# Kernel tuning notes

Hardware: AMD Instinct MI355X
Metric: run time of the kernel (lower is better)

The kernel has to match this reference:

```python
import jax, jax.numpy as jnp
import numpy as np

B, T, DIM, FF, E, TOPK = 2, 2048, 1024, 4096, 8, 2


def setup_inputs() -> dict:
    key = jax.random.key(0)
    k0, k1, k2, k3 = jax.random.split(key, 4)
    x = jax.random.normal(k0, (B, T, DIM), jnp.float32)
    # router weight [E, D] (nn.Linear(dim, num_experts, bias=False))
    Wr = jax.random.normal(k1, (E, DIM), jnp.float32) * (DIM ** -0.5)
    # per-expert FFN weights, stacked: W1 [E, D, FF], W2 [E, FF, D]
    W1 = jax.random.normal(k2, (E, DIM, FF), jnp.float32) * (DIM ** -0.5)
    W2 = jax.random.normal(k3, (E, FF, DIM), jnp.float32) * (FF ** -0.5)
    return {"x": x, "Wr": Wr, "W1": W1, "W2": W2}


def reference(x, Wr, W1, W2):
    """MoEFeedForward.forward, world_size=1, STANDARD implementation.

    Math: per token, top_k experts by router logits, softmax over the top_k
    logits (fp32), y = sum_k w_k * FFN_{e_k}(x). The torch code realizes this
    via sort/permute + per-expert variable-size GEMM + weighted index_add;
    the scatter-add result is identical to the dense masked form below,
    which is the jit-friendly (static-shape) expression.
    """
    Bn, Tn, D = x.shape
    num_experts = Wr.shape[0]
    xf = x.reshape(-1, D)                      # [N, D], N = B*T
    N = xf.shape[0]

    logits = xf @ Wr.T                         # [N, E]
    topw, topi = jax.lax.top_k(logits, TOPK)   # [N, K]
    topw = jax.nn.softmax(topw.astype(jnp.float32), axis=-1).astype(x.dtype)

    # combine weight for each (token, expert): [N, E] (0 if not routed)
    combine = jnp.zeros((N, num_experts), x.dtype)
    combine = combine.at[jnp.arange(N)[:, None], topi].add(topw)

    out = jnp.zeros_like(xf)
    for e in range(num_experts):               # fixed small loop over experts
        h = jax.nn.gelu(xf @ W1[e], approximate=False)  # exact GELU (nn.GELU)
        out = out + combine[:, e:e + 1] * (h @ W2[e])
    return out.reshape(Bn, Tn, D)
```

## Files before the change

### kernel.cpp

```cpp
#include <hip/hip_runtime.h>
#include <hip/hip_bf16.h>
#include <hip/hip_fp16.h>

#define NTOK 4096
#define DIM 1024
#define FF 4096
#define NE 8
#define NSLOT 8192

typedef _Float16 half8 __attribute__((ext_vector_type(8)));
typedef _Float16 half4 __attribute__((ext_vector_type(4)));
typedef float floatx4 __attribute__((ext_vector_type(4)));

__device__ __forceinline__ float gelu_exact(float x) {
    return 0.5f * x * (1.0f + erff(x * 0.70710678118654752f));
}

__device__ __forceinline__ void gl_lds16(const void* g, void* l) {
    __builtin_amdgcn_global_load_lds(
        (const __attribute__((address_space(1))) void*)g,
        (__attribute__((address_space(3))) void*)l, 16, 0, 0);
}

__global__ __launch_bounds__(256) void k_convert_x(const float* __restrict__ x,
                                                   _Float16* __restrict__ xh) {
    int i = (blockIdx.x * 256 + threadIdx.x) * 8;
    float4 a = *(const float4*)(x + i);
    float4 b = *(const float4*)(x + i + 4);
    half8 h;
    h[0] = (_Float16)a.x; h[1] = (_Float16)a.y; h[2] = (_Float16)a.z; h[3] = (_Float16)a.w;
    h[4] = (_Float16)b.x; h[5] = (_Float16)b.y; h[6] = (_Float16)b.z; h[7] = (_Float16)b.w;
    *(half8*)(xh + i) = h;
}

template<typename LdsT>
__device__ __forceinline__ void transpose_tile(const float* __restrict__ s,
                                               _Float16* __restrict__ d,
                                               int R, int C, int r0, int c0,
                                               LdsT* ldsraw) {
    float (*t)[65] = (float (*)[65])ldsraw;
    int tid = threadIdx.x;
    int rr = tid >> 4, cc = (tid & 15) * 4;
#pragma unroll
    for (int i = 0; i < 4; ++i) {
        float4 v = *(const float4*)(s + (size_t)(r0 + rr + i * 16) * C + c0 + cc);
        t[rr + i * 16][cc] = v.x; t[rr + i * 16][cc + 1] = v.y;
        t[rr + i * 16][cc + 2] = v.z; t[rr + i * 16][cc + 3] = v.w;
    }
    __syncthreads();
    int f = tid >> 3, ch = tid & 7;
#pragma unroll
    for (int j = 0; j < 2; ++j) {
        int fr = f + j * 32;
        half8 v;
#pragma unroll
        for (int u = 0; u < 8; ++u) v[u] = (_Float16)t[ch * 8 + u][fr];
        *(half8*)(d + (size_t)(c0 + fr) * R + r0 + ch * 8) = v;
    }
}

__global__ __launch_bounds__(256) void k_transpose(const float* __restrict__ src,
                                                   _Float16* __restrict__ dst,
                                                   int R, int C) {
    __shared__ float t[64][65];
    int e = blockIdx.z;
    transpose_tile(src + (size_t)e * R * C, dst + (size_t)e * C * R,
                   R, C, blockIdx.y * 64, blockIdx.x * 64, &t[0][0]);
}

__global__ __launch_bounds__(256) void k_router(const float* __restrict__ x,
                                                const float* __restrict__ Wr,
                                                int* __restrict__ counts,
                                                int* __restrict__ tok_e,
                                                float* __restrict__ tok_w,
                                                int* __restrict__ tok_pos) {
    __shared__ float wr[NE * DIM];
    int tid = threadIdx.x;
    for (int i = tid; i < NE * DIM / 4; i += 256)
        ((float4*)wr)[i] = ((const float4*)Wr)[i];
    __syncthreads();

    int w = tid >> 6, lane = tid & 63;
    int t = blockIdx.x * 4 + w;

    float acc[NE] = {};
    for (int j = 0; j < DIM / 64; ++j) {
        float xv = x[t * DIM + j * 64 + lane];
#pragma unroll
        for (int e = 0; e < NE; ++e)
            acc[e] += xv * wr[e * DIM + j * 64 + lane];
    }
#pragma unroll
    for (int e = 0; e < NE; ++e) {
#pragma unroll
        for (int s = 32; s; s >>= 1) acc[e] += __shfl_xor(acc[e], s, 64);
    }
    if (lane == 0) {
        int b0 = 0; float m0 = acc[0];
#pragma unroll
        for (int e = 1; e < NE; ++e) { if (acc[e] > m0) { m0 = acc[e]; b0 = e; } }
        int b1 = -1; float m1 = -1e30f;
#pragma unroll
        for (int e = 0; e < NE; ++e) { if (e != b0 && acc[e] > m1) { m1 = acc[e]; b1 = e; } }
        float z = __expf(m1 - m0);
        float zz = 1.0f / (1.0f + z);
        int p0 = atomicAdd(&counts[b0], 1);
        int p1 = atomicAdd(&counts[b1], 1);
        tok_e[2 * t] = b0;  tok_e[2 * t + 1] = b1;
        tok_w[2 * t] = zz;  tok_w[2 * t + 1] = z * zz;
        tok_pos[2 * t] = p0; tok_pos[2 * t + 1] = p1;
    }
}

__global__ void k_prefix(const int* __restrict__ counts, int* __restrict__ offs,
                         int* __restrict__ tmap256, int* __restrict__ tmap128) {
    if (threadIdx.x == 0 && blockIdx.x == 0) {
        int s = 0, n2 = 0, n1 = 0;
        for (int e = 0; e < NE; ++e) {
            offs[e] = s;
            int c = counts[e];
            for (int mt = 0; mt * 256 < c; ++mt) tmap256[1 + n2++] = (e << 16) | mt;
            for (int mt = 0; mt * 128 < c; ++mt) tmap128[1 + n1++] = (e << 16) | mt;
            s += c;
        }
        offs[NE] = s;
        tmap256[0] = n2;
        tmap128[0] = n1;
    }
}

__global__ __launch_bounds__(256) void k_slots(const int* __restrict__ offs,
                                               const int* __restrict__ tok_e,
                                               const int* __restrict__ tok_pos,
                                               int* __restrict__ tok_slot,
                                               int* __restrict__ list_tok) {
    int idx = blockIdx.x * 256 + threadIdx.x;
    if (idx < NSLOT) {
        int e = tok_e[idx];
        int slot = offs[e] + tok_pos[idx];
        tok_slot[idx] = slot;
        list_tok[slot] = idx >> 1;
    }
}

template<int K, int NOUT, bool GATHER, bool GELU>
__device__ __forceinline__ void ffn128_body(
    const _Float16* __restrict__ Abase,
    const _Float16* __restrict__ Wbase,
    const int* __restrict__ counts,
    const int* __restrict__ offs,
    const int* __restrict__ list_tok,
    _Float16* __restrict__ Out,
    int e, int mt, int f0, _Float16* lds) {

    int base = offs[e] + mt * 128;
    int valid = counts[e] - mt * 128;

    int tid = threadIdx.x;
    int wid = tid >> 6, lane = tid & 63;

    const char* AB = (const char*)Abase;
    const char* WB = (const char*)(Wbase + (size_t)e * NOUT * K);

    size_t aoff[4]; unsigned boff[4];
#pragma unroll
    for (int i = 0; i < 4; ++i) {
        int g = wid * 256 + i * 64 + lane;
        int r = g >> 3;
        int c = (g & 7) ^ (r & 7);
        int rr = (r < valid) ? r : (valid - 1);
        unsigned arow = GATHER ? (unsigned)list_tok[base + rr] : (unsigned)(base + rr);
        aoff[i] = (size_t)arow * (K * 2) + c * 16;
        boff[i] = (unsigned)(f0 + r) * (unsigned)(K * 2) + c * 16;
    }

    floatx4 acc[4][4];
#pragma unroll
    for (int m = 0; m < 4; ++m)
#pragma unroll
        for (int n = 0; n < 4; ++n) acc[m][n] = (floatx4){0.f, 0.f, 0.f, 0.f};

    int la = lane & 15, lb = lane >> 4;
    int wm = (wid >> 1) * 64, wn = (wid & 1) * 64;

#pragma unroll
    for (int i = 0; i < 4; ++i)
        gl_lds16(AB + aoff[i], lds + wid * 2048 + i * 512);
#pragma unroll
    for (int i = 0; i < 4; ++i)
        gl_lds16(WB + boff[i], lds + 16384 + wid * 2048 + i * 512);
    asm volatile("s_waitcnt vmcnt(0)" ::: "memory");
    __builtin_amdgcn_s_barrier();
    __builtin_amdgcn_sched_barrier(0);

    constexpr int NT = K / 64;
#pragma unroll 2
    for (int t = 0; t < NT; ++t) {
        int cur = t & 1;
        if (t + 1 < NT) {
            size_t kadv = (size_t)(t + 1) * 128;
            _Float16* Ad = lds + (cur ^ 1) * 8192;
            _Float16* Bd = lds + 16384 + (cur ^ 1) * 8192;
#pragma unroll
            for (int i = 0; i < 4; ++i)
                gl_lds16(AB + aoff[i] + kadv, Ad + wid * 2048 + i * 512);
#pragma unroll
            for (int i = 0; i < 4; ++i)
                gl_lds16(WB + boff[i] + kadv, Bd + wid * 2048 + i * 512);
        }
        const _Float16* Ac = lds + cur * 8192;
        const _Float16* Bc = lds + 16384 + cur * 8192;
#pragma unroll
        for (int kk = 0; kk < 2; ++kk) {
            half8 af[4], bf[4];
#pragma unroll
            for (int m = 0; m < 4; ++m) {
                int row = wm + m * 16 + la;
                int c = kk * 4 + lb;
                af[m] = *(const half8*)(Ac + row * 64 + ((c ^ (row & 7)) * 8));
            }
#pragma unroll
            for (int n = 0; n < 4; ++n) {
                int row = wn + n * 16 + la;
                int c = kk * 4 + lb;
                bf[n] = *(const half8*)(Bc + row * 64 + ((c ^ (row & 7)) * 8));
            }
#pragma unroll
            for (int m = 0; m < 4; ++m)
#pragma unroll
                for (int n = 0; n < 4; ++n)
                    acc[m][n] = __builtin_amdgcn_mfma_f32_16x16x32_f16(af[m], bf[n], acc[m][n], 0, 0, 0);
        }
        __builtin_amdgcn_sched_barrier(0);
        asm volatile("s_waitcnt vmcnt(0)" ::: "memory");
        __builtin_amdgcn_s_barrier();
        __builtin_amdgcn_sched_barrier(0);
    }

    _Float16* tw = lds + wid * 4096;
#pragma unroll
    for (int m = 0; m < 4; ++m)
#pragma unroll
        for (int n = 0; n < 4; ++n) {
            floatx4 v = acc[m][n];
#pragma unroll
            for (int i = 0; i < 4; ++i) {
                float fv = v[i];
                if (GELU) fv = gelu_exact(fv);
                tw[(m * 16 + lb * 4 + i) * 64 + n * 16 + la] = (_Float16)fv;
            }
        }
    asm volatile("s_waitcnt lgkmcnt(0)" ::: "memory");
    __builtin_amdgcn_sched_barrier(0);
#pragma unroll
    for (int i = 0; i < 8; ++i) {
        int gi = i * 64 + lane;
        int row = gi >> 3, c8 = gi & 7;
        half8 v = *(const half8*)(tw + gi * 8);
        int trow = wm + row;
        if (trow < valid)
            *(half8*)(Out + (size_t)(base + trow) * NOUT + f0 + wn + c8 * 8) = v;
    }
}

template<int K, int NOUT, bool GATHER, bool GELU>
__global__ __launch_bounds__(256) void k_ffn(
    const _Float16* __restrict__ Abase,
    const _Float16* __restrict__ Wbase,
    const int* __restrict__ tmap,
    const int* __restrict__ counts,
    const int* __restrict__ offs,
    const int* __restrict__ list_tok,
    _Float16* __restrict__ Out) {
    __shared__ _Float16 lds[32768];
    int nt_m = tmap[0];
    if ((int)blockIdx.x >= nt_m) return;
    int ent = tmap[1 + blockIdx.x];
    ffn128_body<K, NOUT, GATHER, GELU>(Abase, Wbase, counts, offs, list_tok, Out,
                                       ent >> 16, ent & 0xffff, blockIdx.y * 128, lds);
}

__global__ __launch_bounds__(256) void k_ffn1_fused(
    const _Float16* __restrict__ xh,
    const _Float16* __restrict__ w1t,
    const int* __restrict__ tmap,
    const int* __restrict__ counts,
    const int* __restrict__ offs,
    const int* __restrict__ list_tok,
    _Float16* __restrict__ hbuf,
    const float* __restrict__ W2,
    _Float16* __restrict__ w2t) {
    __shared__ _Float16 lds[32768];
    int bid = blockIdx.x;
    int q = bid / 9, r = bid % 9;
    if (r < 2) {
        int f = q * 2 + r;
        int nt_m = tmap[0];
        int tile = f >> 5;
        if (tile >= nt_m) return;
        int ent = tmap[1 + tile];
        ffn128_body<DIM, FF, true, true>(xh, w1t, counts, offs, list_tok, hbuf,
                                         ent >> 16, ent & 0xffff, (f & 31) * 128, lds);
    } else {
        int t = q * 7 + (r - 2);
        if (t >= 16 * 64 * NE) return;
        int e = t >> 10, rem = t & 1023;
        int cx = rem & 15, ry = rem >> 4;
        transpose_tile(W2 + (size_t)e * FF * DIM, w2t + (size_t)e * DIM * FF,
                       FF, DIM, ry * 64, cx * 64, (float*)lds);
    }
}

template<int K, int NOUT, int KSPAN, bool GATHER, bool GELU>
__global__ __launch_bounds__(512, 2) void k_ffn256(
    const _Float16* __restrict__ Abase,
    const _Float16* __restrict__ Wbase,
    const int* __restrict__ tmap,
    const int* __restrict__ counts,
    const int* __restrict__ offs,
    const int* __restrict__ list_tok,
    _Float16* __restrict__ Out) {

    int nt_m = tmap[0];
    if ((int)blockIdx.x >= nt_m) return;
    int ent = tmap[1 + blockIdx.x];
    int e = ent >> 16, mt = ent & 0xffff;
    int base = offs[e] + mt * 256;
    int valid = counts[e] - mt * 256;
    int f0 = blockIdx.y * 256;
    int kbase = blockIdx.z * KSPAN;
    Out += (size_t)blockIdx.z * ((size_t)NSLOT * NOUT);

    __shared__ _Float16 lds[65536];

    int tid = threadIdx.x;
    int wid = tid >> 6, lane = tid & 63;

    const char* AB = (const char*)Abase;
    const char* WB = (const char*)(Wbase + (size_t)e * NOUT * K);

    size_t aoff[4]; unsigned boff[4];
#pragma unroll
    for (int i = 0; i < 4; ++i) {
        int g = i * 512 + tid;
        int r = g >> 3;
        int c = (g & 7) ^ (r & 7);
        int rr = (r < valid) ? r : (valid - 1);
        unsigned arow = GATHER ? (unsigned)list_tok[base + rr] : (unsigned)(base + rr);
        aoff[i] = (size_t)arow * (K * 2) + c * 16 + (size_t)kbase * 2;
        boff[i] = (unsigned)(f0 + r) * (unsigned)(K * 2) + c * 16 + (unsigned)kbase * 2;
    }

    floatx4 acc[8][4];
#pragma unroll
    for (int m = 0; m < 8; ++m)
#pragma unroll
        for (int n = 0; n < 4; ++n) acc[m][n] = (floatx4){0.f, 0.f, 0.f, 0.f};

    int la = lane & 15, lb = lane >> 4;
    int wmb = (wid >> 2) * 128, wnb = (wid & 3) * 64;

#pragma unroll
    for (int i = 0; i < 4; ++i)
        gl_lds16(AB + aoff[i], lds + i * 4096 + wid * 512);
#pragma unroll
    for (int i = 0; i < 4; ++i)
        gl_lds16(WB + boff[i], lds + 32768 + i * 4096 + wid * 512);
    asm volatile("s_waitcnt vmcnt(0)" ::: "memory");
    __builtin_amdgcn_s_barrier();
    __builtin_amdgcn_sched_barrier(0);

    constexpr int NT = KSPAN / 64;
#pragma unroll 2
    for (int t = 0; t < NT; ++t) {
        int cur = t & 1;
        if (t + 1 < NT) {
            size_t adv = (size_t)(t + 1) * 128;
            _Float16* Ad = lds + (cur ^ 1) * 16384;
            _Float16* Bd = lds + 32768 + (cur ^ 1) * 16384;
#pragma unroll
            for (int i = 0; i < 4; ++i)
                gl_lds16(AB + aoff[i] + adv, Ad + i * 4096 + wid * 512);
#pragma unroll
            for (int i = 0; i < 4; ++i)
                gl_lds16(WB + boff[i] + adv, Bd + i * 4096 + wid * 512);
        }
        const _Float16* Ac = lds + cur * 16384;
        const _Float16* Bc = lds + 32768 + cur * 16384;
#pragma unroll
        for (int kk = 0; kk < 2; ++kk) {
            half8 af[8], bf[4];
#pragma unroll
            for (int n = 0; n < 4; ++n) {
                int row = wnb + n * 16 + la;
                int c = kk * 4 + lb;
                bf[n] = *(const half8*)(Bc + row * 64 + ((c ^ (row & 7)) * 8));
            }
#pragma unroll
            for (int m = 0; m < 8; ++m) {
                int row = wmb + m * 16 + la;
                int c = kk * 4 + lb;
                af[m] = *(const half8*)(Ac + row * 64 + ((c ^ (row & 7)) * 8));
            }
#pragma unroll
            for (int m = 0; m < 8; ++m)
#pragma unroll
                for (int n = 0; n < 4; ++n)
                    acc[m][n] = __builtin_amdgcn_mfma_f32_16x16x32_f16(af[m], bf[n], acc[m][n], 0, 0, 0);
        }
        __builtin_amdgcn_sched_barrier(0);
        asm volatile("s_waitcnt vmcnt(0)" ::: "memory");
        __builtin_amdgcn_s_barrier();
        __builtin_amdgcn_sched_barrier(0);
    }

    _Float16* tw = lds + wid * 4096;
#pragma unroll
    for (int ps = 0; ps < 2; ++ps) {
#pragma unroll
        for (int fi = 0; fi < 4; ++fi)
#pragma unroll
            for (int nf = 0; nf < 4; ++nf) {
                floatx4 v = acc[ps * 4 + fi][nf];
#pragma unroll
                for (int i2 = 0; i2 < 4; ++i2) {
                    float fv = v[i2];
                    if (GELU) fv = gelu_exact(fv);
                    tw[(fi * 16 + lb * 4 + i2) * 64 + nf * 16 + la] = (_Float16)fv;
                }
            }
        asm volatile("s_waitcnt lgkmcnt(0)" ::: "memory");
        __builtin_amdgcn_sched_barrier(0);
#pragma unroll
        for (int i2 = 0; i2 < 8; ++i2) {
            int gi = i2 * 64 + lane;
            int row = gi >> 3, c8 = gi & 7;
            half8 v = *(const half8*)(tw + gi * 8);
            int trow = wmb + ps * 64 + row;
            if (trow < valid)
                *(half8*)(Out + (size_t)(base + trow) * NOUT + f0 + wnb + c8 * 8) = v;
        }
    }
}

__global__ __launch_bounds__(256) void k_combine(const _Float16* __restrict__ yp,
                                                 const int* __restrict__ tok_slot,
                                                 const float* __restrict__ tok_w,
                                                 float* __restrict__ out,
                                                 int nsplit) {
    int t = blockIdx.x;
    int d = threadIdx.x * 4;
    int s0 = tok_slot[2 * t], s1 = tok_slot[2 * t + 1];
    float w0 = tok_w[2 * t], w1 = tok_w[2 * t + 1];
    float4 sum0 = {0.f, 0.f, 0.f, 0.f}, sum1 = {0.f, 0.f, 0.f, 0.f};
    for (int z = 0; z < nsplit; ++z) {
        const _Float16* p = yp + (size_t)z * NSLOT * DIM;
        half4 y0 = *(const half4*)(p + (size_t)s0 * DIM + d);
        half4 y1 = *(const half4*)(p + (size_t)s1 * DIM + d);
        sum0.x += (float)y0[0]; sum0.y += (float)y0[1];
        sum0.z += (float)y0[2]; sum0.w += (float)y0[3];
        sum1.x += (float)y1[0]; sum1.y += (float)y1[1];
        sum1.z += (float)y1[2]; sum1.w += (float)y1[3];
    }
    float4 o;
    o.x = w0 * sum0.x + w1 * sum1.x;
    o.y = w0 * sum0.y + w1 * sum1.y;
    o.z = w0 * sum0.z + w1 * sum1.z;
    o.w = w0 * sum0.w + w1 * sum1.w;
    *(float4*)(out + (size_t)t * DIM + d) = o;
}

extern "C" void kernel_launch(void* const* d_in, const int* in_sizes, int n_in,
                              void* d_out, int out_size, void* d_ws, size_t ws_size,
                              hipStream_t stream) {
    const float* x  = (const float*)d_in[0];
    const float* Wr = (const float*)d_in[1];
    const float* W1 = (const float*)d_in[2];
    const float* W2 = (const float*)d_in[3];
    float* out = (float*)d_out;

    char* ws = (char*)d_ws;
    _Float16* w1t  = (_Float16*)ws;
    _Float16* xh   = (_Float16*)(ws + 67108864);
    _Float16* hbuf = (_Float16*)(ws + 75497472);
    char* p = ws + 142606336;
    int*   counts   = (int*)p;        p += 1024;
    int*   offs     = (int*)p;        p += 1024;
    int*   tmap256  = (int*)p;        p += 1024;
    int*   tmap128  = (int*)p;        p += 1024;
    int*   tok_e    = (int*)p;        p += NSLOT * 4;
    float* tok_w    = (float*)p;      p += NSLOT * 4;
    int*   tok_pos  = (int*)p;        p += NSLOT * 4;
    int*   tok_slot = (int*)p;        p += NSLOT * 4;
    int*   list_tok = (int*)p;        p += NSLOT * 4;
    const size_t OFF_EXT = 142606336 + 196608;
    const size_t SZ_Y  = (size_t)NSLOT * DIM * 2;
    const size_t SZ_WT = (size_t)NE * DIM * FF * 2;

    bool fused = (ws_size >= OFF_EXT + SZ_WT);

    hipMemsetAsync(counts, 0, NE * sizeof(int), stream);
    k_convert_x<<<NTOK * DIM / (256 * 8), 256, 0, stream>>>(x, xh);
    k_router<<<NTOK / 4, 256, 0, stream>>>(x, Wr, counts, tok_e, tok_w, tok_pos);
    k_prefix<<<1, 64, 0, stream>>>(counts, offs, tmap256, tmap128);
    k_slots<<<NSLOT / 256, 256, 0, stream>>>(offs, tok_e, tok_pos, tok_slot, list_tok);
    k_transpose<<<dim3(FF / 64, DIM / 64, NE), 256, 0, stream>>>(W1, w1t, DIM, FF);

    if (fused) {
        _Float16* w2t = (_Float16*)(ws + OFF_EXT);
        _Float16* yp  = (_Float16*)ws;
        k_ffn1_fused<<<9 * 1171, 256, 0, stream>>>(
            xh, w1t, tmap128, counts, offs, list_tok, hbuf, W2, w2t);
        k_ffn256<FF, DIM, 1024, false, false>
            <<<dim3(NSLOT / 256 + NE, DIM / 256, 4), 512, 0, stream>>>(
                hbuf, w2t, tmap256, counts, offs, list_tok, yp);
        k_combine<<<NTOK, 256, 0, stream>>>(yp, tok_slot, tok_w, out, 4);
    } else {
        _Float16* w2t = w1t;
        _Float16* yp  = (_Float16*)(ws + OFF_EXT);
        int nsplit = (ws_size >= OFF_EXT + 2 * SZ_Y) ? 2 : 1;
        k_ffn<DIM, FF, true, true>
            <<<dim3(NSLOT / 128 + NE, FF / 128), 256, 0, stream>>>(
                xh, w1t, tmap128, counts, offs, list_tok, hbuf);
        k_transpose<<<dim3(DIM / 64, FF / 64, NE), 256, 0, stream>>>(W2, w2t, FF, DIM);
        if (nsplit == 2) {
            k_ffn256<FF, DIM, 2048, false, false>
                <<<dim3(NSLOT / 256 + NE, DIM / 256, 2), 512, 0, stream>>>(
                    hbuf, w2t, tmap256, counts, offs, list_tok, yp);
        } else {
            k_ffn<FF, DIM, false, false>
                <<<dim3(NSLOT / 128 + NE, DIM / 128), 256, 0, stream>>>(
                    hbuf, w2t, tmap128, counts, offs, list_tok, yp);
        }
        k_combine<<<NTOK, 256, 0, stream>>>(yp, tok_slot, tok_w, out, nsplit);
    }
}
```

Measured before the change: 408.5 us.

## Merge routing and prep kernels and use 128x64 transpose tiles

The x conversion, router and W1 transpose now run as one interleaved `k_prep` launch. Prefix and slot assignment become a single one-block kernel. The W1 and W2 transpose tiles grow from 64x64 to 128x64, and the fused FFN1/W2-transpose grid is re-split as 2 GEMM slots to 8 transpose slots out of every 10 blocks. The aim is fewer kernel launches and less per-tile transpose overhead, and the fused kernels overlap dissimilar work. In exchange, `k_prep` needs 33 KB of shared memory per block, which may lower occupancy, and slot assignment now runs serially in a single block.

```diff
diff --git a/kernel.cpp b/kernel.cpp
--- a/kernel.cpp
+++ b/kernel.cpp
@@ -22,40 +22,93 @@
         (__attribute__((address_space(3))) void*)l, 16, 0, 0);
 }
 
-__global__ __launch_bounds__(256) void k_convert_x(const float* __restrict__ x,
-                                                   _Float16* __restrict__ xh) {
-    int i = (blockIdx.x * 256 + threadIdx.x) * 8;
-    float4 a = *(const float4*)(x + i);
-    float4 b = *(const float4*)(x + i + 4);
-    half8 h;
-    h[0] = (_Float16)a.x; h[1] = (_Float16)a.y; h[2] = (_Float16)a.z; h[3] = (_Float16)a.w;
-    h[4] = (_Float16)b.x; h[5] = (_Float16)b.y; h[6] = (_Float16)b.z; h[7] = (_Float16)b.w;
-    *(half8*)(xh + i) = h;
-}
-
-template<typename LdsT>
-__device__ __forceinline__ void transpose_tile(const float* __restrict__ s,
-                                               _Float16* __restrict__ d,
-                                               int R, int C, int r0, int c0,
-                                               LdsT* ldsraw) {
-    float (*t)[65] = (float (*)[65])ldsraw;
+__device__ __forceinline__ void transpose_tile128(const float* __restrict__ s,
+                                                  _Float16* __restrict__ d,
+                                                  int R, int C, int r0, int c0,
+                                                  char* smem) {
+    float (*t)[66] = (float (*)[66])smem;
     int tid = threadIdx.x;
     int rr = tid >> 4, cc = (tid & 15) * 4;
 #pragma unroll
-    for (int i = 0; i < 4; ++i) {
+    for (int i = 0; i < 8; ++i) {
         float4 v = *(const float4*)(s + (size_t)(r0 + rr + i * 16) * C + c0 + cc);
         t[rr + i * 16][cc] = v.x; t[rr + i * 16][cc + 1] = v.y;
         t[rr + i * 16][cc + 2] = v.z; t[rr + i * 16][cc + 3] = v.w;
     }
     __syncthreads();
-    int f = tid >> 3, ch = tid & 7;
-#pragma unroll
-    for (int j = 0; j < 2; ++j) {
-        int fr = f + j * 32;
+#pragma unroll
+    for (int j = 0; j < 4; ++j) {
+        int chunk = j * 256 + tid;
+        int fr = chunk >> 4, ch = chunk & 15;
         half8 v;
 #pragma unroll
         for (int u = 0; u < 8; ++u) v[u] = (_Float16)t[ch * 8 + u][fr];
         *(half8*)(d + (size_t)(c0 + fr) * R + r0 + ch * 8) = v;
+    }
+}
+
+__global__ __launch_bounds__(256) void k_prep(
+    const float* __restrict__ x,
+    const float* __restrict__ Wr,
+    const float* __restrict__ W1,
+    _Float16* __restrict__ w1t,
+    _Float16* __restrict__ xh,
+    int* __restrict__ counts,
+    int* __restrict__ tok_e,
+    float* __restrict__ tok_w,
+    int* __restrict__ tok_pos) {
+    __shared__ char smem[33792];
+    int bid = blockIdx.x;
+    int q = bid / 7, r = bid % 7;
+    int tid = threadIdx.x;
+    if (r < 4) {
+        int t = q * 4 + r;
+        int e = t >> 9, rem = t & 511;
+        int r0 = (rem >> 6) << 7, c0 = (rem & 63) << 6;
+        transpose_tile128(W1 + (size_t)e * DIM * FF, w1t + (size_t)e * FF * DIM,
+                          DIM, FF, r0, c0, smem);
+    } else if (r < 6) {
+        int i = (q * 2 + (r - 4)) * 2048 + tid * 8;
+        float4 a = *(const float4*)(x + i);
+        float4 b = *(const float4*)(x + i + 4);
+        half8 h;
+        h[0] = (_Float16)a.x; h[1] = (_Float16)a.y; h[2] = (_Float16)a.z; h[3] = (_Float16)a.w;
+        h[4] = (_Float16)b.x; h[5] = (_Float16)b.y; h[6] = (_Float16)b.z; h[7] = (_Float16)b.w;
+        *(half8*)(xh + i) = h;
+    } else {
+        float* wr = (float*)smem;
+        for (int i = tid; i < NE * DIM / 4; i += 256)
+            ((float4*)wr)[i] = ((const float4*)Wr)[i];
+        __syncthreads();
+        int w = tid >> 6, lane = tid & 63;
+        int t = q * 4 + w;
+        float acc[NE] = {};
+        for (int j = 0; j < DIM / 64; ++j) {
+            float xv = x[t * DIM + j * 64 + lane];
+#pragma unroll
+            for (int e = 0; e < NE; ++e)
+                acc[e] += xv * wr[e * DIM + j * 64 + lane];
+        }
+#pragma unroll
+        for (int e = 0; e < NE; ++e) {
+#pragma unroll
+            for (int s = 32; s; s >>= 1) acc[e] += __shfl_xor(acc[e], s, 64);
+        }
+        if (lane == 0) {
+            int b0 = 0; float m0 = acc[0];
+#pragma unroll
+            for (int e = 1; e < NE; ++e) { if (acc[e] > m0) { m0 = acc[e]; b0 = e; } }
+            int b1 = -1; float m1 = -1e30f;
+#pragma unroll
+            for (int e = 0; e < NE; ++e) { if (e != b0 && acc[e] > m1) { m1 = acc[e]; b1 = e; } }
+            float z = __expf(m1 - m0);
+            float zz = 1.0f / (1.0f + z);
+            int p0 = atomicAdd(&counts[b0], 1);
+            int p1 = atomicAdd(&counts[b1], 1);
+            tok_e[2 * t] = b0;  tok_e[2 * t + 1] = b1;
+            tok_w[2 * t] = zz;  tok_w[2 * t + 1] = z * zz;
+            tok_pos[2 * t] = p0; tok_pos[2 * t + 1] = p1;
+        }
     }
 }
 
@@ -64,60 +117,39 @@
                                                    int R, int C) {
     __shared__ float t[64][65];
     int e = blockIdx.z;
-    transpose_tile(src + (size_t)e * R * C, dst + (size_t)e * C * R,
-                   R, C, blockIdx.y * 64, blockIdx.x * 64, &t[0][0]);
-}
-
-__global__ __launch_bounds__(256) void k_router(const float* __restrict__ x,
-                                                const float* __restrict__ Wr,
-                                                int* __restrict__ counts,
-                                                int* __restrict__ tok_e,
-                                                float* __restrict__ tok_w,
-                                                int* __restrict__ tok_pos) {
-    __shared__ float wr[NE * DIM];
+    const float* s = src + (size_t)e * R * C;
+    _Float16* d = dst + (size_t)e * C * R;
+    int r0 = blockIdx.y * 64, c0 = blockIdx.x * 64;
     int tid = threadIdx.x;
-    for (int i = tid; i < NE * DIM / 4; i += 256)
-        ((float4*)wr)[i] = ((const float4*)Wr)[i];
+    int rr = tid >> 4, cc = (tid & 15) * 4;
+#pragma unroll
+    for (int i = 0; i < 4; ++i) {
+        float4 v = *(const float4*)(s + (size_t)(r0 + rr + i * 16) * C + c0 + cc);
+        t[rr + i * 16][cc] = v.x; t[rr + i * 16][cc + 1] = v.y;
+        t[rr + i * 16][cc + 2] = v.z; t[rr + i * 16][cc + 3] = v.w;
+    }
     __syncthreads();
-
-    int w = tid >> 6, lane = tid & 63;
-    int t = blockIdx.x * 4 + w;
-
-    float acc[NE] = {};
-    for (int j = 0; j < DIM / 64; ++j) {
-        float xv = x[t * DIM + j * 64 + lane];
-#pragma unroll
-        for (int e = 0; e < NE; ++e)
-            acc[e] += xv * wr[e * DIM + j * 64 + lane];
-    }
-#pragma unroll
-    for (int e = 0; e < NE; ++e) {
-#pragma unroll
-        for (int s = 32; s; s >>= 1) acc[e] += __shfl_xor(acc[e], s, 64);
-    }
-    if (lane == 0) {
-        int b0 = 0; float m0 = acc[0];
-#pragma unroll
-        for (int e = 1; e < NE; ++e) { if (acc[e] > m0) { m0 = acc[e]; b0 = e; } }
-        int b1 = -1; float m1 = -1e30f;
-#pragma unroll
-        for (int e = 0; e < NE; ++e) { if (e != b0 && acc[e] > m1) { m1 = acc[e]; b1 = e; } }
-        float z = __expf(m1 - m0);
-        float zz = 1.0f / (1.0f + z);
-        int p0 = atomicAdd(&counts[b0], 1);
-        int p1 = atomicAdd(&counts[b1], 1);
-        tok_e[2 * t] = b0;  tok_e[2 * t + 1] = b1;
-        tok_w[2 * t] = zz;  tok_w[2 * t + 1] = z * zz;
-        tok_pos[2 * t] = p0; tok_pos[2 * t + 1] = p1;
-    }
-}
-
-__global__ void k_prefix(const int* __restrict__ counts, int* __restrict__ offs,
-                         int* __restrict__ tmap256, int* __restrict__ tmap128) {
-    if (threadIdx.x == 0 && blockIdx.x == 0) {
+    int f = tid >> 3, ch = tid & 7;
+#pragma unroll
+    for (int j = 0; j < 2; ++j) {
+        int fr = f + j * 32;
+        half8 v;
+#pragma unroll
+        for (int u = 0; u < 8; ++u) v[u] = (_Float16)t[ch * 8 + u][fr];
+        *(half8*)(d + (size_t)(c0 + fr) * R + r0 + ch * 8) = v;
+    }
+}
+
+__global__ __launch_bounds__(256) void k_prefix_slots(
+    const int* __restrict__ counts, int* __restrict__ offs,
+    int* __restrict__ tmap256, int* __restrict__ tmap128,
+    const int* __restrict__ tok_e, const int* __restrict__ tok_pos,
+    int* __restrict__ tok_slot, int* __restrict__ list_tok) {
+    __shared__ int soffs[NE];
+    if (threadIdx.x == 0) {
         int s = 0, n2 = 0, n1 = 0;
         for (int e = 0; e < NE; ++e) {
-            offs[e] = s;
+            offs[e] = s; soffs[e] = s;
             int c = counts[e];
             for (int mt = 0; mt * 256 < c; ++mt) tmap256[1 + n2++] = (e << 16) | mt;
             for (int mt = 0; mt * 128 < c; ++mt) tmap128[1 + n1++] = (e << 16) | mt;
@@ -127,17 +159,10 @@
         tmap256[0] = n2;
         tmap128[0] = n1;
     }
-}
-
-__global__ __launch_bounds__(256) void k_slots(const int* __restrict__ offs,
-                                               const int* __restrict__ tok_e,
-                                               const int* __restrict__ tok_pos,
-                                               int* __restrict__ tok_slot,
-                                               int* __restrict__ list_tok) {
-    int idx = blockIdx.x * 256 + threadIdx.x;
-    if (idx < NSLOT) {
+    __syncthreads();
+    for (int idx = threadIdx.x; idx < NSLOT; idx += 256) {
         int e = tok_e[idx];
-        int slot = offs[e] + tok_pos[idx];
+        int slot = soffs[e] + tok_pos[idx];
         tok_slot[idx] = slot;
         list_tok[slot] = idx >> 1;
     }
@@ -292,7 +317,7 @@
     _Float16* __restrict__ w2t) {
     __shared__ _Float16 lds[32768];
     int bid = blockIdx.x;
-    int q = bid / 9, r = bid % 9;
+    int q = bid / 10, r = bid % 10;
     if (r < 2) {
         int f = q * 2 + r;
         int nt_m = tmap[0];
@@ -302,12 +327,12 @@
         ffn128_body<DIM, FF, true, true>(xh, w1t, counts, offs, list_tok, hbuf,
                                          ent >> 16, ent & 0xffff, (f & 31) * 128, lds);
     } else {
-        int t = q * 7 + (r - 2);
-        if (t >= 16 * 64 * NE) return;
-        int e = t >> 10, rem = t & 1023;
-        int cx = rem & 15, ry = rem >> 4;
-        transpose_tile(W2 + (size_t)e * FF * DIM, w2t + (size_t)e * DIM * FF,
-                       FF, DIM, ry * 64, cx * 64, (float*)lds);
+        int t = q * 8 + (r - 2);
+        if (t >= 8 * 32 * 16) return;
+        int e = t >> 9, rem = t & 511;
+        int r0 = (rem >> 4) << 7, c0 = (rem & 15) << 6;
+        transpose_tile128(W2 + (size_t)e * FF * DIM, w2t + (size_t)e * DIM * FF,
+                          FF, DIM, r0, c0, (char*)lds);
     }
 }
 
@@ -500,16 +525,15 @@
     bool fused = (ws_size >= OFF_EXT + SZ_WT);
 
     hipMemsetAsync(counts, 0, NE * sizeof(int), stream);
-    k_convert_x<<<NTOK * DIM / (256 * 8), 256, 0, stream>>>(x, xh);
-    k_router<<<NTOK / 4, 256, 0, stream>>>(x, Wr, counts, tok_e, tok_w, tok_pos);
-    k_prefix<<<1, 64, 0, stream>>>(counts, offs, tmap256, tmap128);
-    k_slots<<<NSLOT / 256, 256, 0, stream>>>(offs, tok_e, tok_pos, tok_slot, list_tok);
-    k_transpose<<<dim3(FF / 64, DIM / 64, NE), 256, 0, stream>>>(W1, w1t, DIM, FF);
+    k_prep<<<7 * 1024, 256, 0, stream>>>(x, Wr, W1, w1t, xh,
+                                         counts, tok_e, tok_w, tok_pos);
+    k_prefix_slots<<<1, 256, 0, stream>>>(counts, offs, tmap256, tmap128,
+                                          tok_e, tok_pos, tok_slot, list_tok);
 
     if (fused) {
         _Float16* w2t = (_Float16*)(ws + OFF_EXT);
         _Float16* yp  = (_Float16*)ws;
-        k_ffn1_fused<<<9 * 1171, 256, 0, stream>>>(
+        k_ffn1_fused<<<10 * 1152, 256, 0, stream>>>(
             xh, w1t, tmap128, counts, offs, list_tok, hbuf, W2, w2t);
         k_ffn256<FF, DIM, 1024, false, false>
             <<<dim3(NSLOT / 256 + NE, DIM / 256, 4), 512, 0, stream>>>(
```

Result: faster. 372.6 us (-8.8%).
